# Kernel tuning notes

Hardware: AMD Instinct MI355X
Metric: run time of the kernel (lower is better)

Reference implementation:

```python
import jax, jax.numpy as jnp
import numpy as np

B, R, P, DP, DR, N, RK = 4, 256, 64, 384, 512, 48, 24


def _ln(x, w, b, eps=1e-5):
    m = x.mean(-1, keepdims=True)
    v = ((x - m) ** 2).mean(-1, keepdims=True)
    return (x - m) / jnp.sqrt(v + eps) * w + b


def _l2norm(x, eps=1e-6):
    return x / jnp.maximum(jnp.linalg.norm(x, axis=-1, keepdims=True), eps)


def setup_inputs() -> dict:
    key = jax.random.key(0)
    ks = jax.random.split(key, 16)
    s = 0.02
    rnd = lambda k, shp: jax.random.normal(k, shp, jnp.float32) * s
    inp = {
        'patch_tokens': jax.random.normal(ks[0], (B, R, P, DP), jnp.float32),
        'patch_mask': jax.random.randint(ks[1], (B, R, P), 0, 2) > 0,
        'near_mask': jax.random.randint(ks[2], (R, R), 0, 2) > 0,
        'far_mask': jax.random.randint(ks[3], (R, R), 0, 2) > 0,
        'local_pos': rnd(ks[4], (1, 1, P, DP)),
        'gate_ln_w': jnp.ones(DP), 'gate_ln_b': jnp.zeros(DP),
        'gate_w1': rnd(ks[5], (DP, DR)), 'gate_b1': jnp.zeros(DR),
        'gate_w2': rnd(ks[6], (DR, 1)), 'gate_b2': jnp.zeros(1),
        'proj_ln1_w': jnp.ones(DP), 'proj_ln1_b': jnp.zeros(DP),
        'proj_w1': rnd(ks[7], (DP, DR)), 'proj_b1': jnp.zeros(DR),
        'proj_w2': rnd(ks[8], (DR, DR)), 'proj_b2': jnp.zeros(DR),
        'proj_ln2_w': jnp.ones(DR), 'proj_ln2_b': jnp.zeros(DR),
        'in_proj_w': rnd(ks[9], (DR, 2 * DR)),
        'x_proj_w': rnd(ks[10], (DR, RK + 2 * N)),
        'dt_w': rnd(ks[11], (RK, DR)),
        'dt_b': jax.random.uniform(ks[12], (DR,), jnp.float32, -4.0, -2.0),
        'A_log': jnp.tile(jnp.log(jnp.arange(1, N + 1, dtype=jnp.float32))[None, :], (DR, 1)),
        'D_param': jnp.ones(DR),
        'out_proj_w': rnd(ks[13], (DR, DR)),
        'scan_ln_w': jnp.ones(DR), 'scan_ln_b': jnp.zeros(DR),
    }
    return inp


def _forward(patch_tokens, patch_mask, near_mask, far_mask, local_pos,
             gate_ln_w, gate_ln_b, gate_w1, gate_b1, gate_w2, gate_b2,
             proj_ln1_w, proj_ln1_b, proj_w1, proj_b1, proj_w2, proj_b2,
             proj_ln2_w, proj_ln2_b, in_proj_w, x_proj_w, dt_w, dt_b,
             A_log, D_param, out_proj_w, scan_ln_w, scan_ln_b):
    # ---- GatedRegionAggregator ----
    x = patch_tokens + local_pos  # [B,R,P,DP]
    g = _ln(x, gate_ln_w, gate_ln_b)
    g = jax.nn.gelu(g @ gate_w1 + gate_b1, approximate=False)
    logits = (g @ gate_w2 + gate_b2)[..., 0]  # [B,R,P]
    logits = jnp.where(patch_mask, logits, jnp.finfo(logits.dtype).min)
    attn = jax.nn.softmax(logits, axis=-1) * patch_mask
    attn = attn / jnp.maximum(attn.sum(-1, keepdims=True), 1e-6)
    pooled = jnp.einsum('brp,brpd->brd', attn, x)  # [B,R,DP]
    p = _ln(pooled, proj_ln1_w, proj_ln1_b)
    p = jax.nn.gelu(p @ proj_w1 + proj_b1, approximate=False)
    p = _ln(p @ proj_w2 + proj_b2, proj_ln2_w, proj_ln2_b)
    p = jnp.nan_to_num(p, nan=0.0, posinf=1.0, neginf=-1.0)
    region = _l2norm(p)  # [B,R,DR]

    # ---- SlowSelectiveScan1D over region sequence (L = R) ----
    xz = region @ in_proj_w  # [B,L,2*DR]
    u, z = jnp.split(xz, 2, axis=-1)
    prm = u @ x_proj_w  # [B,L,RK+2N]
    dt_raw, Bm, Cm = prm[..., :RK], prm[..., RK:RK + N], prm[..., RK + N:]
    delta = jnp.minimum(jax.nn.softplus(dt_raw @ dt_w + dt_b), 10.0)  # [B,L,DR]
    A = -jnp.minimum(jnp.exp(A_log), 1e4)  # [DR,N]
    dA = jnp.exp(jnp.clip(delta[..., None] * A[None, None], -30.0, 30.0))  # [B,L,DR,N]
    dBu = delta[..., None] * Bm[:, :, None, :] * u[..., None]  # [B,L,DR,N]
    log_cumA = jnp.cumsum(jnp.log(jnp.maximum(dA, 1e-38)), axis=1)
    h = jnp.exp(log_cumA) * jnp.cumsum(dBu * jnp.exp(-log_cumA), axis=1)
    y_seq = jnp.einsum('bln,bldn->bld', Cm, h) + D_param * u
    y = (y_seq * jax.nn.silu(z)) @ out_proj_w
    out = _ln(region + jnp.nan_to_num(y, nan=0.0, posinf=1.0, neginf=-1.0),
              scan_ln_w, scan_ln_b)  # [B,R,DR]

    # ---- topology_loss_static ----
    rt = _l2norm(out.astype(jnp.float32))
    sim = jnp.einsum('brd,bsd->brs', rt, rt)  # [B,R,R]
    near = near_mask.astype(sim.dtype)[None]
    far = far_mask.astype(sim.dtype)[None]
    near_loss = ((1.0 - sim) * near).sum() / jnp.maximum(near.sum(), 1.0)
    far_loss = (jax.nn.relu(sim - 0.2) * far).sum() / jnp.maximum(far.sum(), 1.0)
    return out, near_loss + far_loss


def reference(patch_tokens, patch_mask, near_mask, far_mask, local_pos,
              gate_ln_w, gate_ln_b, gate_w1, gate_b1, gate_w2, gate_b2,
              proj_ln1_w, proj_ln1_b, proj_w1, proj_b1, proj_w2, proj_b2,
              proj_ln2_w, proj_ln2_b, in_proj_w, x_proj_w, dt_w, dt_b,
              A_log, D_param, out_proj_w, scan_ln_w, scan_ln_b):
    return _forward(patch_tokens, patch_mask, near_mask, far_mask, local_pos,
                    gate_ln_w, gate_ln_b, gate_w1, gate_b1, gate_w2, gate_b2,
                    proj_ln1_w, proj_ln1_b, proj_w1, proj_b1, proj_w2, proj_b2,
                    proj_ln2_w, proj_ln2_b, in_proj_w, x_proj_w, dt_w, dt_b,
                    A_log, D_param, out_proj_w, scan_ln_w, scan_ln_b)
```

## Files before the change

### kernel.cpp

```cpp
#include <hip/hip_runtime.h>
#include <hip/hip_bf16.h>
#include <math.h>

#define B_ 4
#define R_ 256
#define P_ 64
#define DP_ 384
#define DR_ 512
#define N_ 48
#define RK_ 24
#define MROWS (B_*R_*P_)
#define REGS  (B_*R_)

typedef unsigned short ushort_t;
typedef __attribute__((ext_vector_type(8))) short bf16x8;
typedef __attribute__((ext_vector_type(4))) float f32x4;

#define GLOAD16(g, l) __builtin_amdgcn_global_load_lds( \
    (const __attribute__((address_space(1))) unsigned int*)(g), \
    (__attribute__((address_space(3))) unsigned int*)(l), 16, 0, 0)

__device__ __forceinline__ float us2f(unsigned short u){
  union { unsigned int i; float f; } x; x.i = ((unsigned int)u) << 16; return x.f;
}
__device__ __forceinline__ unsigned short f2us(float f){
  __hip_bfloat16 h = __float2bfloat16(f);
  return *reinterpret_cast<unsigned short*>(&h);
}
__device__ __forceinline__ float gelu_f(float x){
  return 0.5f * x * (1.0f + erff(x * 0.70710678118654752f));
}
__device__ __forceinline__ float wred_sum(float v){
#pragma unroll
  for (int m = 1; m < 64; m <<= 1) v += __shfl_xor(v, m, 64);
  return v;
}
__device__ __forceinline__ void block_sum4(float v[4], float* s){
  int lane = threadIdx.x & 63, wid = threadIdx.x >> 6;
#pragma unroll
  for (int i = 0; i < 4; ++i){
    float x = v[i];
#pragma unroll
    for (int m = 1; m < 64; m <<= 1) x += __shfl_xor(x, m, 64);
    if (lane == 0) s[wid * 4 + i] = x;
  }
  __syncthreads();
  if (threadIdx.x < 4){
    float t = 0.f;
    for (int t2 = 0; t2 < 8; ++t2) t += s[t2 * 4 + threadIdx.x];
    s[32 + threadIdx.x] = t;
  }
  __syncthreads();
#pragma unroll
  for (int i = 0; i < 4; ++i) v[i] = s[32 + i];
  __syncthreads();
}
__device__ __forceinline__ void block_sum2(float& a, float& b, float* s){
  int lane = threadIdx.x & 63, wid = threadIdx.x >> 6;
  float x = a, y = b;
#pragma unroll
  for (int m = 1; m < 64; m <<= 1){ x += __shfl_xor(x, m, 64); y += __shfl_xor(y, m, 64); }
  if (lane == 0){ s[wid * 2] = x; s[wid * 2 + 1] = y; }
  __syncthreads();
  if (threadIdx.x < 2){
    float t = 0.f;
    for (int j = 0; j < 8; ++j) t += s[j * 2 + threadIdx.x];
    s[16 + threadIdx.x] = t;
  }
  __syncthreads();
  a = s[16]; b = s[17];
  __syncthreads();
}

__global__ __launch_bounds__(512) void k_prep(
    const float* __restrict__ gw1, const float* __restrict__ glnw,
    const float* __restrict__ glnb, const float* __restrict__ gb1,
    ushort_t* __restrict__ W1pT, float* __restrict__ s1,
    float* __restrict__ b1p, float* __restrict__ accum){
  __shared__ float pss[8][64], psb[8][64];
  int tid = threadIdx.x, seg = tid >> 6, nl = tid & 63;
  int n = blockIdx.x * 64 + nl;
  if (blockIdx.x == 0 && tid < 4) accum[tid] = 0.f;
  float s = 0.f, sb = 0.f;
  int k0 = seg * 48;
  for (int i = 0; i < 48; ++i){
    int k = k0 + i;
    float w1 = gw1[k * DR_ + n];
    float v = glnw[k] * w1;
    unsigned short vr = f2us(v);
    s  += us2f(vr);
    sb += glnb[k] * w1;
    W1pT[(size_t)n * DP_ + k] = vr;
  }
  pss[seg][nl] = s; psb[seg][nl] = sb;
  __syncthreads();
  if (tid < 64){
    float ts = 0.f, tb = 0.f;
    for (int j = 0; j < 8; ++j){ ts += pss[j][tid]; tb += psb[j][tid]; }
    s1[blockIdx.x * 64 + tid] = ts;
    b1p[blockIdx.x * 64 + tid] = gb1[blockIdx.x * 64 + tid] + tb;
  }
}

__global__ __launch_bounds__(512) void k_xform(
    const float* __restrict__ pt, const float* __restrict__ lp,
    ushort_t* __restrict__ xb, float* __restrict__ mu, float* __restrict__ rsg){
  int tid = threadIdx.x, w = tid >> 6, lane = tid & 63;
  size_t r = (size_t)blockIdx.x * 8 + w;
  int p = (int)(r & (P_ - 1));
  const float* xr = pt + r * DP_ + lane * 6;
  const float* lr = lp + (size_t)p * DP_ + lane * 6;
  float x[6];
  float s = 0.f, ss = 0.f;
#pragma unroll
  for (int i = 0; i < 6; i += 2){
    float2 a = *(const float2*)(xr + i);
    float2 b = *(const float2*)(lr + i);
    x[i] = a.x + b.x; x[i + 1] = a.y + b.y;
  }
#pragma unroll
  for (int i = 0; i < 6; ++i){ s += x[i]; ss += x[i] * x[i]; }
  s = wred_sum(s); ss = wred_sum(ss);
  if (lane == 0){
    float m = s * (1.f / DP_);
    float var = ss * (1.f / DP_) - m * m;
    mu[r] = m;
    rsg[r] = rsqrtf(var + 1e-5f);
  }
  ushort_t* xw = xb + r * DP_ + lane * 6;
#pragma unroll
  for (int i = 0; i < 6; i += 2){
    ushort2 u2; u2.x = f2us(x[i]); u2.y = f2us(x[i + 1]);
    *(ushort2*)(xw + i) = u2;
  }
}

__global__ __launch_bounds__(512, 4) void k_gate_pool(
    const ushort_t* __restrict__ xb,
    const ushort_t* __restrict__ BT,
    const float* __restrict__ mu, const float* __restrict__ rsg,
    const float* __restrict__ s1, const float* __restrict__ b1p,
    const float* __restrict__ w2, const int* __restrict__ pmask,
    float* __restrict__ pooled){
  __shared__ __align__(16) ushort_t Abuf[64 * 64];
  __shared__ float logit_lds[64];
  __shared__ float smu[64], srs[64];
  __shared__ float attn[64];
  int tid = threadIdx.x;
  int lane = tid & 63, w = tid >> 6;
  int t = lane & 15, g = lane >> 4;
  long r0 = (long)blockIdx.x * 64;
  if (tid < 64){
    logit_lds[tid] = 0.f;
    smu[tid] = mu[r0 + tid];
    srs[tid] = rsg[r0 + tid];
  }

  f32x4 acc[4][4];
#pragma unroll
  for (int m = 0; m < 4; ++m)
#pragma unroll
    for (int n = 0; n < 4; ++n) acc[m][n] = (f32x4){0.f, 0.f, 0.f, 0.f};

  int arow8 = (w << 3) + (lane >> 3);
  int akc = lane & 7;
  const ushort_t* asrc0 = xb + (size_t)(r0 + arow8) * DP_ + ((akc ^ (arow8 & 7)) << 3);
  ushort_t* adst = Abuf + (w << 9);

  for (int kt = 0; kt < 6; ++kt){
    __syncthreads();
    GLOAD16(asrc0 + kt * 64, adst);
    __syncthreads();
#pragma unroll
    for (int kk = 0; kk < 2; ++kk){
      int ch = kk * 4 + g;
      bf16x8 af[4], bfr[4];
#pragma unroll
      for (int m = 0; m < 4; ++m){
        int row = m * 16 + t;
        af[m] = *(const bf16x8*)(Abuf + row * 64 + ((ch ^ (row & 7)) << 3));
      }
#pragma unroll
      for (int n = 0; n < 4; ++n){
        int rowb = w * 64 + n * 16 + t;
        bfr[n] = *(const bf16x8*)(BT + (size_t)rowb * DP_ + kt * 64 + ch * 8);
      }
#pragma unroll
      for (int m = 0; m < 4; ++m)
#pragma unroll
        for (int n = 0; n < 4; ++n)
          acc[m][n] = __builtin_amdgcn_mfma_f32_16x16x32_bf16(af[m], bfr[n], acc[m][n], 0, 0, 0);
    }
  }
  __syncthreads();

  float w2c[4], s1c[4], b1c[4];
#pragma unroll
  for (int n = 0; n < 4; ++n){
    int c = w * 64 + n * 16 + t;
    w2c[n] = w2[c]; s1c[n] = s1[c]; b1c[n] = b1p[c];
  }
#pragma unroll
  for (int m = 0; m < 4; ++m){
#pragma unroll
    for (int j = 0; j < 4; ++j){
      int rl = m * 16 + g * 4 + j;
      float mur = smu[rl], rs = srs[rl];
      float part = 0.f;
#pragma unroll
      for (int n = 0; n < 4; ++n){
        float gp = rs * acc[m][n][j] - mur * rs * s1c[n] + b1c[n];
        part += gelu_f(gp) * w2c[n];
      }
#pragma unroll
      for (int msk = 1; msk < 16; msk <<= 1) part += __shfl_xor(part, msk, 64);
      if (t == 0) atomicAdd(&logit_lds[rl], part);
    }
  }
  __syncthreads();

  if (tid < 64){
    int mk = pmask[r0 + tid];
    float lv = logit_lds[tid];
    float lm = mk ? lv : -3.4e38f;
    float M = lm;
#pragma unroll
    for (int m2 = 1; m2 < 64; m2 <<= 1) M = fmaxf(M, __shfl_xor(M, m2, 64));
    float e = mk ? __expf(lv - M) : 0.f;
    float S = e;
#pragma unroll
    for (int m2 = 1; m2 < 64; m2 <<= 1) S += __shfl_xor(S, m2, 64);
    float a = (S > 0.f) ? e / S : 0.f;
    float S2 = a;
#pragma unroll
    for (int m2 = 1; m2 < 64; m2 <<= 1) S2 += __shfl_xor(S2, m2, 64);
    attn[tid] = a / fmaxf(S2, 1e-6f);
  }
  __syncthreads();

  if (tid < DP_){
    float accp = 0.f;
#pragma unroll 4
    for (int p = 0; p < P_; ++p)
      accp += attn[p] * us2f(xb[(size_t)(r0 + p) * DP_ + tid]);
    pooled[(long)blockIdx.x * DP_ + tid] = accp;
  }
}

__global__ __launch_bounds__(512) void k_region(
    const float* __restrict__ pooled,
    const float* __restrict__ ln1w, const float* __restrict__ ln1b,
    const float* __restrict__ pw1, const float* __restrict__ pb1,
    const float* __restrict__ pw2, const float* __restrict__ pb2,
    const float* __restrict__ ln2w, const float* __restrict__ ln2b,
    const float* __restrict__ inpw, const float* __restrict__ xpw,
    const float* __restrict__ dtw, const float* __restrict__ dtb,
    float* __restrict__ region, float* __restrict__ uT, float* __restrict__ zT,
    float* __restrict__ deltaT, float* __restrict__ BmT, float* __restrict__ CmT){
  __shared__ float xr[2][DP_];
  __shared__ float p1[2][DR_];
  __shared__ float rg[2][DR_];
  __shared__ float us[2][DR_];
  __shared__ float ps[4][2][128];
  __shared__ float prm[2][RK_ + 2 * N_];
  __shared__ float red[24];
  int tid = threadIdx.x;
  int r0 = blockIdx.x * 2;
  for (int i = tid; i < 2 * DP_; i += 512) xr[i / DP_][i % DP_] = pooled[(long)r0 * DP_ + i];
  __syncthreads();
  float v0 = (tid < DP_) ? xr[0][tid] : 0.f;
  float v1 = (tid < DP_) ? xr[1][tid] : 0.f;
  float s0 = v0, s1v = v1;
  block_sum2(s0, s1v, red);
  float dv0 = (tid < DP_) ? (v0 - s0 * (1.f / DP_)) : 0.f;
  float dv1 = (tid < DP_) ? (v1 - s1v * (1.f / DP_)) : 0.f;
  float q0 = dv0 * dv0, q1 = dv1 * dv1;
  block_sum2(q0, q1, red);
  if (tid < DP_){
    float lw = ln1w[tid], lb = ln1b[tid];
    xr[0][tid] = dv0 * rsqrtf(q0 * (1.f / DP_) + 1e-5f) * lw + lb;
    xr[1][tid] = dv1 * rsqrtf(q1 * (1.f / DP_) + 1e-5f) * lw + lb;
  }
  __syncthreads();
  {
    float pb = pb1[tid];
    float a0 = pb, a1 = pb;
    for (int k0 = 0; k0 < DP_; k0 += 8){
      float wv[8];
#pragma unroll
      for (int j = 0; j < 8; ++j) wv[j] = pw1[(k0 + j) * DR_ + tid];
#pragma unroll
      for (int j = 0; j < 8; ++j){
        a0 = fmaf(xr[0][k0 + j], wv[j], a0);
        a1 = fmaf(xr[1][k0 + j], wv[j], a1);
      }
    }
    p1[0][tid] = gelu_f(a0); p1[1][tid] = gelu_f(a1);
  }
  __syncthreads();
  float qq0, qq1;
  {
    float pb = pb2[tid];
    float a0 = pb, a1 = pb;
    for (int k0 = 0; k0 < DR_; k0 += 8){
      float wv[8];
#pragma unroll
      for (int j = 0; j < 8; ++j) wv[j] = pw2[(k0 + j) * DR_ + tid];
#pragma unroll
      for (int j = 0; j < 8; ++j){
        a0 = fmaf(p1[0][k0 + j], wv[j], a0);
        a1 = fmaf(p1[1][k0 + j], wv[j], a1);
      }
    }
    qq0 = a0; qq1 = a1;
  }
  {
    float m0 = qq0, m1 = qq1;
    block_sum2(m0, m1, red);
    float d0 = qq0 - m0 * (1.f / DR_), d1 = qq1 - m1 * (1.f / DR_);
    float w0 = d0 * d0, w1 = d1 * d1;
    block_sum2(w0, w1, red);
    float lw = ln2w[tid], lb = ln2b[tid];
    float o0 = d0 * rsqrtf(w0 * (1.f / DR_) + 1e-5f) * lw + lb;
    float o1 = d1 * rsqrtf(w1 * (1.f / DR_) + 1e-5f) * lw + lb;
    if (isnan(o0)) o0 = 0.f; else if (isinf(o0)) o0 = (o0 > 0.f) ? 1.f : -1.f;
    if (isnan(o1)) o1 = 0.f; else if (isinf(o1)) o1 = (o1 > 0.f) ? 1.f : -1.f;
    float n0 = o0 * o0, n1 = o1 * o1;
    block_sum2(n0, n1, red);
    float r0v = o0 / fmaxf(sqrtf(n0), 1e-6f);
    float r1v = o1 / fmaxf(sqrtf(n1), 1e-6f);
    rg[0][tid] = r0v; rg[1][tid] = r1v;
    region[(long)r0 * DR_ + tid] = r0v;
    region[(long)(r0 + 1) * DR_ + tid] = r1v;
  }
  __syncthreads();
  {
    float ua0 = 0.f, ua1 = 0.f, zb0 = 0.f, zb1 = 0.f;
    for (int k0 = 0; k0 < DR_; k0 += 8){
      float w1v[8], w2v[8];
#pragma unroll
      for (int j = 0; j < 8; ++j){
        w1v[j] = inpw[(k0 + j) * 1024 + tid];
        w2v[j] = inpw[(k0 + j) * 1024 + tid + 512];
      }
#pragma unroll
      for (int j = 0; j < 8; ++j){
        float x0 = rg[0][k0 + j], x1 = rg[1][k0 + j];
        ua0 = fmaf(x0, w1v[j], ua0); ua1 = fmaf(x1, w1v[j], ua1);
        zb0 = fmaf(x0, w2v[j], zb0); zb1 = fmaf(x1, w2v[j], zb1);
      }
    }
    us[0][tid] = ua0; us[1][tid] = ua1;
    uT[(long)tid * REGS + r0] = ua0;
    uT[(long)tid * REGS + r0 + 1] = ua1;
    zT[(long)tid * REGS + r0] = zb0;
    zT[(long)tid * REGS + r0 + 1] = zb1;
  }
  __syncthreads();
  {
    int sseg = tid >> 7, c = tid & 127;
    float pr0 = 0.f, pr1 = 0.f;
    if (c < RK_ + 2 * N_){
      int kb = sseg * 128;
      for (int k0 = kb; k0 < kb + 128; k0 += 8){
        float wv[8];
#pragma unroll
        for (int j = 0; j < 8; ++j) wv[j] = xpw[(k0 + j) * (RK_ + 2 * N_) + c];
#pragma unroll
        for (int j = 0; j < 8; ++j){
          pr0 = fmaf(us[0][k0 + j], wv[j], pr0);
          pr1 = fmaf(us[1][k0 + j], wv[j], pr1);
        }
      }
    }
    ps[sseg][0][c] = pr0; ps[sseg][1][c] = pr1;
  }
  __syncthreads();
  if (tid < 256){
    int rr2 = tid >> 7, cc = tid & 127;
    if (cc < RK_ + 2 * N_)
      prm[rr2][cc] = ps[0][rr2][cc] + ps[1][rr2][cc] + ps[2][rr2][cc] + ps[3][rr2][cc];
  }
  __syncthreads();
#pragma unroll
  for (int r = 0; r < 2; ++r){
    float aa = dtb[tid];
#pragma unroll
    for (int j = 0; j < RK_; ++j) aa = fmaf(prm[r][j], dtw[j * DR_ + tid], aa);
    float sp = (aa > 20.f) ? aa : log1pf(expf(aa));
    deltaT[(long)tid * REGS + r0 + r] = fminf(sp, 10.f);
  }
  if (tid < N_){
#pragma unroll
    for (int r = 0; r < 2; ++r){
      BmT[(long)tid * REGS + r0 + r] = prm[r][RK_ + tid];
      CmT[(long)tid * REGS + r0 + r] = prm[r][RK_ + N_ + tid];
    }
  }
}

__global__ __launch_bounds__(256) void k_scan(
    const float* __restrict__ deltaT, const float* __restrict__ uT,
    const float* __restrict__ zT, const float* __restrict__ BmT,
    const float* __restrict__ CmT, const float* __restrict__ alog,
    const float* __restrict__ Dp, float* __restrict__ ys){
  __shared__ float sAn[N_];
  __shared__ float sA[N_][4];
  __shared__ float sB[N_][4];
  int tid = threadIdx.x, lane = tid & 63, w = tid >> 6;
  int ch = blockIdx.x;
  int b = ch >> 9, d = ch & (DR_ - 1);
  if (tid < N_) sAn[tid] = -fminf(__expf(alog[d * N_ + tid]), 10000.f);
  long col = (long)b * R_ + tid;
  float dl = deltaT[(long)d * REGS + col];
  float uu = uT[(long)d * REGS + col];
  float zz = zT[(long)d * REGS + col];
  float Dd = Dp[d];
  float part = 0.f;
  __syncthreads();
  for (int nc = 0; nc < 6; ++nc){
    float bmv[8], cmv[8];
#pragma unroll
    for (int j = 0; j < 8; ++j){
      bmv[j] = BmT[(long)(nc * 8 + j) * REGS + col];
      cmv[j] = CmT[(long)(nc * 8 + j) * REGS + col];
    }
    float aA[8], aB[8];
#pragma unroll
    for (int j = 0; j < 8; ++j){
      int n = nc * 8 + j;
      float cc = fminf(fmaxf(dl * sAn[n], -30.f), 30.f);
      float a = exp2f(cc * 1.44269504f);
      float bv = dl * bmv[j] * uu;
#pragma unroll
      for (int s = 1; s < 64; s <<= 1){
        float a_sh = __shfl_up(a, (unsigned)s, 64);
        float b_sh = __shfl_up(bv, (unsigned)s, 64);
        float nb = fmaf(a, b_sh, bv);
        float na = a * a_sh;
        if (lane >= s){ bv = nb; a = na; }
      }
      aA[j] = a; aB[j] = bv;
      if (lane == 63){ sA[n][w] = a; sB[n][w] = bv; }
    }
    __syncthreads();
#pragma unroll
    for (int j = 0; j < 8; ++j){
      int n = nc * 8 + j;
      float hin = 0.f;
#pragma unroll
      for (int tt = 0; tt < 3; ++tt){
        if (tt < w) hin = sA[n][tt] * hin + sB[n][tt];
      }
      float h = fmaf(aA[j], hin, aB[j]);
      part = fmaf(cmv[j], h, part);
    }
    if (nc < 5) __syncthreads();
  }
  float yv = part + Dd * uu;
  float sz = zz / (1.f + __expf(-zz));
  ys[col * DR_ + d] = yv * sz;
}

__global__ __launch_bounds__(512) void k_out(
    const float* __restrict__ ys, const float* __restrict__ W,
    const float* __restrict__ region, const float* __restrict__ lnw,
    const float* __restrict__ lnb, float* __restrict__ outp,
    float* __restrict__ rt){
  __shared__ float yr[4][DR_];
  __shared__ float red[40];
  int tid = threadIdx.x;
  int r0 = blockIdx.x * 4;
  for (int i = tid; i < 4 * DR_; i += 512) yr[i >> 9][i & 511] = ys[(long)r0 * DR_ + i];
  __syncthreads();
  float y[4] = {0,0,0,0};
  for (int k0 = 0; k0 < DR_; k0 += 8){
    float wv[8];
#pragma unroll
    for (int j = 0; j < 8; ++j) wv[j] = W[(k0 + j) * DR_ + tid];
#pragma unroll
    for (int j = 0; j < 8; ++j){
#pragma unroll
      for (int i = 0; i < 4; ++i) y[i] = fmaf(yr[i][k0 + j], wv[j], y[i]);
    }
  }
  float v[4], t4[4];
#pragma unroll
  for (int i = 0; i < 4; ++i){
    if (isnan(y[i])) y[i] = 0.f; else if (isinf(y[i])) y[i] = (y[i] > 0.f) ? 1.f : -1.f;
    v[i] = region[(long)(r0 + i) * DR_ + tid] + y[i];
    t4[i] = v[i];
  }
  block_sum4(t4, red);
  float dv[4];
#pragma unroll
  for (int i = 0; i < 4; ++i){ dv[i] = v[i] - t4[i] * (1.f / DR_); t4[i] = dv[i] * dv[i]; }
  block_sum4(t4, red);
  float o[4];
  float lw = lnw[tid], lb = lnb[tid];
#pragma unroll
  for (int i = 0; i < 4; ++i){
    o[i] = dv[i] * rsqrtf(t4[i] * (1.f / DR_) + 1e-5f) * lw + lb;
    outp[(long)(r0 + i) * DR_ + tid] = o[i];
    t4[i] = o[i] * o[i];
  }
  block_sum4(t4, red);
#pragma unroll
  for (int i = 0; i < 4; ++i)
    rt[(long)(r0 + i) * DR_ + tid] = o[i] / fmaxf(sqrtf(t4[i]), 1e-6f);
}

__global__ __launch_bounds__(512) void k_loss(
    const float* __restrict__ rt, const int* __restrict__ nearm,
    const int* __restrict__ farm, float* __restrict__ accum){
  __shared__ __align__(16) float ar[4][DR_];
  __shared__ float ps[2][4][256];
  __shared__ float wsum[8][4];
  int blk = blockIdx.x, tid = threadIdx.x;
  int b = blk >> 6, q0 = (blk & 63) * 4;
  const float* rtb = rt + (long)b * R_ * DR_;
  for (int i = tid; i < 4 * DR_; i += 512) ar[i >> 9][i & 511] = rtb[(long)q0 * DR_ + i];
  __syncthreads();
  int s = tid & 255, h = tid >> 8;
  const float* rsrow = rtb + (long)s * DR_ + h * 256;
  float dq[4] = {0.f, 0.f, 0.f, 0.f};
  for (int k = 0; k < 256; k += 4){
    float4 yv = *(const float4*)(rsrow + k);
#pragma unroll
    for (int q = 0; q < 4; ++q){
      float4 x = *(const float4*)(&ar[q][h * 256 + k]);
      dq[q] += x.x * yv.x + x.y * yv.y + x.z * yv.z + x.w * yv.w;
    }
  }
#pragma unroll
  for (int q = 0; q < 4; ++q) ps[h][q][s] = dq[q];
  __syncthreads();
  float nl = 0.f, fl = 0.f, nc = 0.f, fc = 0.f;
  if (tid < 256){
#pragma unroll
    for (int q = 0; q < 4; ++q){
      float dot = ps[0][q][tid] + ps[1][q][tid];
      int nm = nearm[(q0 + q) * R_ + tid], fm = farm[(q0 + q) * R_ + tid];
      if (nm){ nl += 1.f - dot; if (b == 0) nc += 1.f; }
      if (fm){ fl += fmaxf(dot - 0.2f, 0.f); if (b == 0) fc += 1.f; }
    }
  }
  nl = wred_sum(nl); fl = wred_sum(fl); nc = wred_sum(nc); fc = wred_sum(fc);
  int w = tid >> 6, lane = tid & 63;
  if (lane == 0){ wsum[w][0] = nl; wsum[w][1] = fl; wsum[w][2] = nc; wsum[w][3] = fc; }
  __syncthreads();
  if (tid == 0){
    float a0 = 0, a1 = 0, a2 = 0, a3 = 0;
    for (int i = 0; i < 8; i++){ a0 += wsum[i][0]; a1 += wsum[i][1]; a2 += wsum[i][2]; a3 += wsum[i][3]; }
    atomicAdd(&accum[0], a0); atomicAdd(&accum[1], a1);
    if (b == 0){ atomicAdd(&accum[2], a2); atomicAdd(&accum[3], a3); }
  }
}

__global__ void k_final(const float* __restrict__ accum, float* __restrict__ outp){
  if (threadIdx.x == 0){
    float loss = accum[0] / fmaxf(accum[2], 1.f) + accum[1] / fmaxf(accum[3], 1.f);
    outp[REGS * DR_] = loss;
  }
}

extern "C" void kernel_launch(void* const* d_in, const int* in_sizes, int n_in,
                              void* d_out, int out_size, void* d_ws, size_t ws_size,
                              hipStream_t stream){
  const float* pt    = (const float*)d_in[0];
  const int*   pmask = (const int*)d_in[1];
  const int*   nearm = (const int*)d_in[2];
  const int*   farm  = (const int*)d_in[3];
  const float* lp    = (const float*)d_in[4];
  const float* glnw  = (const float*)d_in[5];
  const float* glnb  = (const float*)d_in[6];
  const float* gw1   = (const float*)d_in[7];
  const float* gb1   = (const float*)d_in[8];
  const float* gw2   = (const float*)d_in[9];
  const float* pln1w = (const float*)d_in[11];
  const float* pln1b = (const float*)d_in[12];
  const float* pw1   = (const float*)d_in[13];
  const float* pb1   = (const float*)d_in[14];
  const float* pw2   = (const float*)d_in[15];
  const float* pb2   = (const float*)d_in[16];
  const float* pln2w = (const float*)d_in[17];
  const float* pln2b = (const float*)d_in[18];
  const float* inpw  = (const float*)d_in[19];
  const float* xpw   = (const float*)d_in[20];
  const float* dtw   = (const float*)d_in[21];
  const float* dtb   = (const float*)d_in[22];
  const float* alog  = (const float*)d_in[23];
  const float* dpar  = (const float*)d_in[24];
  const float* opw   = (const float*)d_in[25];
  const float* slnw  = (const float*)d_in[26];
  const float* slnb  = (const float*)d_in[27];

  char* ws = (char*)d_ws;
  size_t off = 0;
  auto alloc = [&](size_t bytes){ size_t o = off; off += (bytes + 255) & ~(size_t)255; return o; };
  ushort_t* W1pT = (ushort_t*)(ws + alloc((size_t)DR_ * DP_ * 2));
  float* s1     = (float*)(ws + alloc(DR_ * 4));
  float* b1p    = (float*)(ws + alloc(DR_ * 4));
  ushort_t* xb  = (ushort_t*)(ws + alloc((size_t)MROWS * DP_ * 2));
  float* mu     = (float*)(ws + alloc((size_t)MROWS * 4));
  float* rsg    = (float*)(ws + alloc((size_t)MROWS * 4));
  float* pooled = (float*)(ws + alloc((size_t)REGS * DP_ * 4));
  float* region = (float*)(ws + alloc((size_t)REGS * DR_ * 4));
  float* uT     = (float*)(ws + alloc((size_t)REGS * DR_ * 4));
  float* zT     = (float*)(ws + alloc((size_t)REGS * DR_ * 4));
  float* deltaT = (float*)(ws + alloc((size_t)REGS * DR_ * 4));
  float* BmT    = (float*)(ws + alloc((size_t)REGS * N_ * 4));
  float* CmT    = (float*)(ws + alloc((size_t)REGS * N_ * 4));
  float* ys     = (float*)(ws + alloc((size_t)REGS * DR_ * 4));
  float* rt     = (float*)(ws + alloc((size_t)REGS * DR_ * 4));
  float* accum  = (float*)(ws + alloc(4 * 4));

  float* outp = (float*)d_out;

  k_prep<<<dim3(8), dim3(512), 0, stream>>>(gw1, glnw, glnb, gb1, W1pT, s1, b1p, accum);
  k_xform<<<dim3(MROWS / 8), dim3(512), 0, stream>>>(pt, lp, xb, mu, rsg);
  k_gate_pool<<<dim3(REGS), dim3(512), 0, stream>>>(xb, W1pT, mu, rsg, s1, b1p, gw2, pmask, pooled);
  k_region<<<dim3(REGS / 2), dim3(512), 0, stream>>>(pooled, pln1w, pln1b, pw1, pb1, pw2, pb2, pln2w, pln2b,
                                                     inpw, xpw, dtw, dtb, region, uT, zT, deltaT, BmT, CmT);
  k_scan<<<dim3(B_ * DR_), dim3(256), 0, stream>>>(deltaT, uT, zT, BmT, CmT, alog, dpar, ys);
  k_out<<<dim3(REGS / 4), dim3(512), 0, stream>>>(ys, opw, region, slnw, slnb, outp, rt);
  k_loss<<<dim3(REGS / 4), dim3(512), 0, stream>>>(rt, nearm, farm, accum);
  k_final<<<dim3(1), dim3(64), 0, stream>>>(accum, outp);
}
```

Measured before the change: 330.4 us.

## Cast region-MLP weights to bf16 blob and double-buffer gate GEMM A tiles

Adds a cast kernel that packs the region MLP, in_proj, x_proj and dt weights into a single bf16 buffer. k_region now reads these half-width weights with deeper unrolling and a 4-block occupancy hint, which is meant to halve weight traffic in this bandwidth-bound kernel. Separately, k_gate_pool double-buffers its LDS A tile so the next global-to-LDS load overlaps the current MFMA step, and it hoists the B fragment loads. The bf16 weights add rounding error, and the extra launch costs a pass over about 1M weights on every call.

```diff
diff --git a/kernel.cpp b/kernel.cpp
--- a/kernel.cpp
+++ b/kernel.cpp
@@ -19,6 +19,13 @@
 #define GLOAD16(g, l) __builtin_amdgcn_global_load_lds( \
     (const __attribute__((address_space(1))) unsigned int*)(g), \
     (__attribute__((address_space(3))) unsigned int*)(l), 16, 0, 0)
+
+#define OFF_PW1  0
+#define OFF_PW2  196608
+#define OFF_INPW 458752
+#define OFF_XPW  983040
+#define OFF_DTW  1044480
+#define NW_TOT   1056768
 
 __device__ __forceinline__ float us2f(unsigned short u){
   union { unsigned int i; float f; } x; x.i = ((unsigned int)u) << 16; return x.f;
@@ -102,6 +109,23 @@
   }
 }
 
+__global__ __launch_bounds__(512) void k_cast(
+    const float* __restrict__ pw1, const float* __restrict__ pw2,
+    const float* __restrict__ inpw, const float* __restrict__ xpw,
+    const float* __restrict__ dtw, ushort_t* __restrict__ dst){
+  int i = (blockIdx.x * 512 + threadIdx.x) * 4;
+  if (i >= NW_TOT) return;
+  const float* s; int off;
+  if (i < OFF_PW2){ s = pw1; off = OFF_PW1; }
+  else if (i < OFF_INPW){ s = pw2; off = OFF_PW2; }
+  else if (i < OFF_XPW){ s = inpw; off = OFF_INPW; }
+  else if (i < OFF_DTW){ s = xpw; off = OFF_XPW; }
+  else { s = dtw; off = OFF_DTW; }
+  float4 v = *(const float4*)(s + (i - off));
+  ushort_t* d = dst + i;
+  d[0] = f2us(v.x); d[1] = f2us(v.y); d[2] = f2us(v.z); d[3] = f2us(v.w);
+}
+
 __global__ __launch_bounds__(512) void k_xform(
     const float* __restrict__ pt, const float* __restrict__ lp,
     ushort_t* __restrict__ xb, float* __restrict__ mu, float* __restrict__ rsg){
@@ -142,7 +166,7 @@
     const float* __restrict__ s1, const float* __restrict__ b1p,
     const float* __restrict__ w2, const int* __restrict__ pmask,
     float* __restrict__ pooled){
-  __shared__ __align__(16) ushort_t Abuf[64 * 64];
+  __shared__ __align__(16) ushort_t Abuf[2][64 * 64];
   __shared__ float logit_lds[64];
   __shared__ float smu[64], srs[64];
   __shared__ float attn[64];
@@ -165,34 +189,40 @@
   int arow8 = (w << 3) + (lane >> 3);
   int akc = lane & 7;
   const ushort_t* asrc0 = xb + (size_t)(r0 + arow8) * DP_ + ((akc ^ (arow8 & 7)) << 3);
-  ushort_t* adst = Abuf + (w << 9);
+  ushort_t* adst0 = Abuf[0] + (w << 9);
+  ushort_t* adst1 = Abuf[1] + (w << 9);
+
+  GLOAD16(asrc0, adst0);
+  __syncthreads();
 
   for (int kt = 0; kt < 6; ++kt){
-    __syncthreads();
-    GLOAD16(asrc0 + kt * 64, adst);
-    __syncthreads();
+    if (kt < 5) GLOAD16(asrc0 + (kt + 1) * 64, (kt & 1) ? adst0 : adst1);
+    const ushort_t* cbuf = (kt & 1) ? Abuf[1] : Abuf[0];
+    bf16x8 bfr[2][4];
+#pragma unroll
+    for (int kk = 0; kk < 2; ++kk)
+#pragma unroll
+      for (int n = 0; n < 4; ++n){
+        int rowb = w * 64 + n * 16 + t;
+        bfr[kk][n] = *(const bf16x8*)(BT + (size_t)rowb * DP_ + kt * 64 + (kk * 4 + g) * 8);
+      }
 #pragma unroll
     for (int kk = 0; kk < 2; ++kk){
       int ch = kk * 4 + g;
-      bf16x8 af[4], bfr[4];
+      bf16x8 af[4];
 #pragma unroll
       for (int m = 0; m < 4; ++m){
         int row = m * 16 + t;
-        af[m] = *(const bf16x8*)(Abuf + row * 64 + ((ch ^ (row & 7)) << 3));
-      }
-#pragma unroll
-      for (int n = 0; n < 4; ++n){
-        int rowb = w * 64 + n * 16 + t;
-        bfr[n] = *(const bf16x8*)(BT + (size_t)rowb * DP_ + kt * 64 + ch * 8);
+        af[m] = *(const bf16x8*)(cbuf + row * 64 + ((ch ^ (row & 7)) << 3));
       }
 #pragma unroll
       for (int m = 0; m < 4; ++m)
 #pragma unroll
         for (int n = 0; n < 4; ++n)
-          acc[m][n] = __builtin_amdgcn_mfma_f32_16x16x32_bf16(af[m], bfr[n], acc[m][n], 0, 0, 0);
-    }
-  }
-  __syncthreads();
+          acc[m][n] = __builtin_amdgcn_mfma_f32_16x16x32_bf16(af[m], bfr[kk][n], acc[m][n], 0, 0, 0);
+    }
+    __syncthreads();
+  }
 
   float w2c[4], s1c[4], b1c[4];
 #pragma unroll
@@ -247,16 +277,20 @@
   }
 }
 
-__global__ __launch_bounds__(512) void k_region(
+__global__ __launch_bounds__(512, 4) void k_region(
     const float* __restrict__ pooled,
     const float* __restrict__ ln1w, const float* __restrict__ ln1b,
-    const float* __restrict__ pw1, const float* __restrict__ pb1,
-    const float* __restrict__ pw2, const float* __restrict__ pb2,
+    const ushort_t* __restrict__ wblob, const float* __restrict__ pb1,
+    const float* __restrict__ pb2,
     const float* __restrict__ ln2w, const float* __restrict__ ln2b,
-    const float* __restrict__ inpw, const float* __restrict__ xpw,
-    const float* __restrict__ dtw, const float* __restrict__ dtb,
+    const float* __restrict__ dtb,
     float* __restrict__ region, float* __restrict__ uT, float* __restrict__ zT,
     float* __restrict__ deltaT, float* __restrict__ BmT, float* __restrict__ CmT){
+  const ushort_t* pw1b  = wblob + OFF_PW1;
+  const ushort_t* pw2b  = wblob + OFF_PW2;
+  const ushort_t* inpwb = wblob + OFF_INPW;
+  const ushort_t* xpwb  = wblob + OFF_XPW;
+  const ushort_t* dtwb  = wblob + OFF_DTW;
   __shared__ float xr[2][DP_];
   __shared__ float p1[2][DR_];
   __shared__ float rg[2][DR_];
@@ -285,14 +319,15 @@
   {
     float pb = pb1[tid];
     float a0 = pb, a1 = pb;
-    for (int k0 = 0; k0 < DP_; k0 += 8){
-      float wv[8];
-#pragma unroll
-      for (int j = 0; j < 8; ++j) wv[j] = pw1[(k0 + j) * DR_ + tid];
-#pragma unroll
-      for (int j = 0; j < 8; ++j){
-        a0 = fmaf(xr[0][k0 + j], wv[j], a0);
-        a1 = fmaf(xr[1][k0 + j], wv[j], a1);
+    for (int k0 = 0; k0 < DP_; k0 += 16){
+      ushort_t wv[16];
+#pragma unroll
+      for (int j = 0; j < 16; ++j) wv[j] = pw1b[(k0 + j) * DR_ + tid];
+#pragma unroll
+      for (int j = 0; j < 16; ++j){
+        float wf = us2f(wv[j]);
+        a0 = fmaf(xr[0][k0 + j], wf, a0);
+        a1 = fmaf(xr[1][k0 + j], wf, a1);
       }
     }
     p1[0][tid] = gelu_f(a0); p1[1][tid] = gelu_f(a1);
@@ -302,14 +337,15 @@
   {
     float pb = pb2[tid];
     float a0 = pb, a1 = pb;
-    for (int k0 = 0; k0 < DR_; k0 += 8){
-      float wv[8];
-#pragma unroll
-      for (int j = 0; j < 8; ++j) wv[j] = pw2[(k0 + j) * DR_ + tid];
-#pragma unroll
-      for (int j = 0; j < 8; ++j){
-        a0 = fmaf(p1[0][k0 + j], wv[j], a0);
-        a1 = fmaf(p1[1][k0 + j], wv[j], a1);
+    for (int k0 = 0; k0 < DR_; k0 += 16){
+      ushort_t wv[16];
+#pragma unroll
+      for (int j = 0; j < 16; ++j) wv[j] = pw2b[(k0 + j) * DR_ + tid];
+#pragma unroll
+      for (int j = 0; j < 16; ++j){
+        float wf = us2f(wv[j]);
+        a0 = fmaf(p1[0][k0 + j], wf, a0);
+        a1 = fmaf(p1[1][k0 + j], wf, a1);
       }
     }
     qq0 = a0; qq1 = a1;
@@ -337,17 +373,18 @@
   {
     float ua0 = 0.f, ua1 = 0.f, zb0 = 0.f, zb1 = 0.f;
     for (int k0 = 0; k0 < DR_; k0 += 8){
-      float w1v[8], w2v[8];
+      ushort_t w1v[8], w2v[8];
 #pragma unroll
       for (int j = 0; j < 8; ++j){
-        w1v[j] = inpw[(k0 + j) * 1024 + tid];
-        w2v[j] = inpw[(k0 + j) * 1024 + tid + 512];
+        w1v[j] = inpwb[(k0 + j) * 1024 + tid];
+        w2v[j] = inpwb[(k0 + j) * 1024 + tid + 512];
       }
 #pragma unroll
       for (int j = 0; j < 8; ++j){
         float x0 = rg[0][k0 + j], x1 = rg[1][k0 + j];
-        ua0 = fmaf(x0, w1v[j], ua0); ua1 = fmaf(x1, w1v[j], ua1);
-        zb0 = fmaf(x0, w2v[j], zb0); zb1 = fmaf(x1, w2v[j], zb1);
+        float wa = us2f(w1v[j]), wb = us2f(w2v[j]);
+        ua0 = fmaf(x0, wa, ua0); ua1 = fmaf(x1, wa, ua1);
+        zb0 = fmaf(x0, wb, zb0); zb1 = fmaf(x1, wb, zb1);
       }
     }
     us[0][tid] = ua0; us[1][tid] = ua1;
@@ -362,14 +399,15 @@
     float pr0 = 0.f, pr1 = 0.f;
     if (c < RK_ + 2 * N_){
       int kb = sseg * 128;
-      for (int k0 = kb; k0 < kb + 128; k0 += 8){
-        float wv[8];
-#pragma unroll
-        for (int j = 0; j < 8; ++j) wv[j] = xpw[(k0 + j) * (RK_ + 2 * N_) + c];
-#pragma unroll
-        for (int j = 0; j < 8; ++j){
-          pr0 = fmaf(us[0][k0 + j], wv[j], pr0);
-          pr1 = fmaf(us[1][k0 + j], wv[j], pr1);
+      for (int k0 = kb; k0 < kb + 128; k0 += 16){
+        ushort_t wv[16];
+#pragma unroll
+        for (int j = 0; j < 16; ++j) wv[j] = xpwb[(k0 + j) * (RK_ + 2 * N_) + c];
+#pragma unroll
+        for (int j = 0; j < 16; ++j){
+          float wf = us2f(wv[j]);
+          pr0 = fmaf(us[0][k0 + j], wf, pr0);
+          pr1 = fmaf(us[1][k0 + j], wf, pr1);
         }
       }
     }
@@ -386,7 +424,7 @@
   for (int r = 0; r < 2; ++r){
     float aa = dtb[tid];
 #pragma unroll
-    for (int j = 0; j < RK_; ++j) aa = fmaf(prm[r][j], dtw[j * DR_ + tid], aa);
+    for (int j = 0; j < RK_; ++j) aa = fmaf(prm[r][j], us2f(dtwb[j * DR_ + tid]), aa);
     float sp = (aa > 20.f) ? aa : log1pf(expf(aa));
     deltaT[(long)tid * REGS + r0 + r] = fminf(sp, 10.f);
   }
@@ -598,9 +636,10 @@
   char* ws = (char*)d_ws;
   size_t off = 0;
   auto alloc = [&](size_t bytes){ size_t o = off; off += (bytes + 255) & ~(size_t)255; return o; };
-  ushort_t* W1pT = (ushort_t*)(ws + alloc((size_t)DR_ * DP_ * 2));
+  ushort_t* W1pT  = (ushort_t*)(ws + alloc((size_t)DR_ * DP_ * 2));
   float* s1     = (float*)(ws + alloc(DR_ * 4));
   float* b1p    = (float*)(ws + alloc(DR_ * 4));
+  ushort_t* wblob = (ushort_t*)(ws + alloc((size_t)NW_TOT * 2));
   ushort_t* xb  = (ushort_t*)(ws + alloc((size_t)MROWS * DP_ * 2));
   float* mu     = (float*)(ws + alloc((size_t)MROWS * 4));
   float* rsg    = (float*)(ws + alloc((size_t)MROWS * 4));
@@ -618,10 +657,11 @@
   float* outp = (float*)d_out;
 
   k_prep<<<dim3(8), dim3(512), 0, stream>>>(gw1, glnw, glnb, gb1, W1pT, s1, b1p, accum);
+  k_cast<<<dim3((NW_TOT / 4 + 511) / 512), dim3(512), 0, stream>>>(pw1, pw2, inpw, xpw, dtw, wblob);
   k_xform<<<dim3(MROWS / 8), dim3(512), 0, stream>>>(pt, lp, xb, mu, rsg);
   k_gate_pool<<<dim3(REGS), dim3(512), 0, stream>>>(xb, W1pT, mu, rsg, s1, b1p, gw2, pmask, pooled);
-  k_region<<<dim3(REGS / 2), dim3(512), 0, stream>>>(pooled, pln1w, pln1b, pw1, pb1, pw2, pb2, pln2w, pln2b,
-                                                     inpw, xpw, dtw, dtb, region, uT, zT, deltaT, BmT, CmT);
+  k_region<<<dim3(REGS / 2), dim3(512), 0, stream>>>(pooled, pln1w, pln1b, wblob, pb1, pb2, pln2w, pln2b,
+                                                     dtb, region, uT, zT, deltaT, BmT, CmT);
   k_scan<<<dim3(B_ * DR_), dim3(256), 0, stream>>>(deltaT, uT, zT, BmT, CmT, alog, dpar, ys);
   k_out<<<dim3(REGS / 4), dim3(512), 0, stream>>>(ys, opw, region, slnw, slnb, outp, rt);
   k_loss<<<dim3(REGS / 4), dim3(512), 0, stream>>>(rt, nearm, farm, accum);
```

Result: faster. 322.1 us (-2.5%).
